# Kernel tuning notes

Measured on AMD Instinct MI355X. Metric: run time of the kernel, lower is better.

Reference implementation:

```python
import jax, jax.numpy as jnp
import numpy as np

NEG_SLOPE = 0.2
EPS = 1e-16

N_NODES = 10000
N_EDGES = 80000
F_IN = 128
HID = 300
H1 = 5  # first_heads
H3 = 3  # out_head
N_CLASSES = 40


def gat_conv(x, edge_index, W, att_src, att_dst, bias, heads, out_ch, concat):
    """PyG-style GATConv (v1 attention), eval mode (no dropout).

    x: [N, F_in]; edge_index: [2, E] (row 0 = source, row 1 = target),
    self-loops already included. W: [F_in, heads*out_ch];
    att_src/att_dst: [heads, out_ch].
    """
    N = x.shape[0]
    h = (x @ W).reshape(N, heads, out_ch)            # [N, H, C]
    a_src = jnp.einsum('nhc,hc->nh', h, att_src)     # [N, H]
    a_dst = jnp.einsum('nhc,hc->nh', h, att_dst)     # [N, H]
    src, dst = edge_index[0], edge_index[1]
    e = jax.nn.leaky_relu(a_src[src] + a_dst[dst], NEG_SLOPE)  # [E, H]
    # segment softmax over incoming edges of each target node
    m = jax.ops.segment_max(e, dst, num_segments=N)  # [N, H]
    ex = jnp.exp(e - m[dst])
    s = jax.ops.segment_sum(ex, dst, num_segments=N)
    alpha = ex / (s[dst] + EPS)                      # [E, H]
    msg = h[src] * alpha[:, :, None]                 # [E, H, C]
    out = jax.ops.segment_sum(msg, dst, num_segments=N)  # [N, H, C]
    if concat:
        out = out.reshape(N, heads * out_ch)
    else:
        out = out.mean(axis=1)
    return out + bias


def setup_inputs() -> dict:
    key = jax.random.key(0)
    ks = jax.random.split(key, 12)
    glorot = lambda k, shape: jax.random.normal(k, shape, jnp.float32) * np.sqrt(
        2.0 / (shape[0] + shape[-1]))
    x = jax.random.normal(ks[0], (N_NODES, F_IN), jnp.float32)
    edge_index = jax.random.randint(ks[1], (2, N_EDGES), 0, N_NODES, jnp.int64)
    return {
        'x': x,
        'edge_index': edge_index,
        'W1': glorot(ks[2], (F_IN, H1 * HID)),
        'as1': glorot(ks[3], (H1, HID)),
        'ad1': glorot(ks[4], (H1, HID)),
        'b1': jnp.zeros((H1 * HID,), jnp.float32),
        'W2': glorot(ks[5], (H1 * HID, H1 * HID)),
        'as2': glorot(ks[6], (H1, HID)),
        'ad2': glorot(ks[7], (H1, HID)),
        'b2': jnp.zeros((H1 * HID,), jnp.float32),
        'W3': glorot(ks[8], (H1 * HID, H3 * N_CLASSES)),
        'as3': glorot(ks[9], (H3, N_CLASSES)),
        'ad3': glorot(ks[10], (H3, N_CLASSES)),
        'b3': jnp.zeros((N_CLASSES,), jnp.float32),
    }


def reference(x, edge_index, W1, as1, ad1, b1, W2, as2, ad2, b2, W3, as3, ad3, b3):
    N = x.shape[0]
    # PyG GATConv adds self-loops by default
    loops = jnp.arange(N, dtype=edge_index.dtype)
    ei = jnp.concatenate([edge_index, jnp.stack([loops, loops])], axis=1)
    # dropout layers are identity in eval mode
    h = gat_conv(x, ei, W1, as1, ad1, b1, H1, HID, True)
    h = jax.nn.elu(h)
    h2 = gat_conv(h, ei, W2, as2, ad2, b2, H1, HID, True)
    h = jax.nn.elu(h + h2)
    h = gat_conv(h, ei, W3, as3, ad3, b3, H3, N_CLASSES, False)  # [N, n_cls]
    pooled = h.sum(axis=0, keepdims=True)                        # [1, n_cls]
    return (pooled, jax.nn.log_softmax(pooled, axis=1))
```

## Files before the change

### kernel.cpp

```cpp
#include <hip/hip_runtime.h>
#include <hip/hip_bf16.h>
#include <math.h>

#define NN       10000
#define F_IN     128
#define HID      300
#define H1       5
#define H3       3
#define NCLS     40
#define HC1      (H1*HID)
#define KPAD     1536
#define HS12     304
#define NL12     1520
#define HS3      48
#define NL3      144
#define LD3      160
#define NEG_SLOPE 0.2f
#define EPSV     1e-16f

typedef __attribute__((ext_vector_type(8))) short bf16x8;
typedef __attribute__((ext_vector_type(8))) unsigned short u16x8;
typedef __attribute__((ext_vector_type(4))) float f32x4;

__device__ inline unsigned short f2bf(float f) {
  unsigned int u = __builtin_bit_cast(unsigned int, f);
  unsigned int r = (u + 0x7FFFu + ((u >> 16) & 1u)) >> 16;
  return (unsigned short)r;
}
__device__ inline float bf2f(unsigned short s) {
  unsigned int u = ((unsigned int)s) << 16;
  return __builtin_bit_cast(float, u);
}

__device__ __forceinline__ void gl2lds16(const unsigned short* g, unsigned short* l) {
  __builtin_amdgcn_global_load_lds(
      (const __attribute__((address_space(1))) unsigned int*)(const void*)g,
      (__attribute__((address_space(3))) unsigned int*)(void*)l, 16, 0, 0);
}

__global__ void k_count(const int* __restrict__ ei, int* __restrict__ counts,
                        int E0, int Etot) {
  int e = blockIdx.x * 256 + threadIdx.x;
  if (e >= Etot) return;
  int dst = (e < E0) ? ei[E0 + e] : (e - E0);
  atomicAdd(&counts[dst], 1);
}

__global__ __launch_bounds__(256) void k_scan(const int* __restrict__ counts,
                                              int* __restrict__ offsets,
                                              int* __restrict__ cursor,
                                              int N, int Etot) {
  __shared__ int sh[256];
  const int CH = 40;
  int t = threadIdx.x;
  int base = t * CH;
  int s = 0;
  for (int i = 0; i < CH; i++) {
    int idx = base + i;
    if (idx < N) s += counts[idx];
  }
  sh[t] = s;
  __syncthreads();
  for (int d = 1; d < 256; d <<= 1) {
    int v = (t >= d) ? sh[t - d] : 0;
    __syncthreads();
    sh[t] += v;
    __syncthreads();
  }
  int run = sh[t] - s;
  for (int i = 0; i < CH; i++) {
    int idx = base + i;
    if (idx < N) {
      offsets[idx] = run;
      cursor[idx] = run;
      run += counts[idx];
    }
  }
  if (t == 0) offsets[N] = Etot;
}

__global__ void k_scatter(const int* __restrict__ ei, int* __restrict__ cursor,
                          int* __restrict__ csr_src, int E0, int Etot) {
  int e = blockIdx.x * 256 + threadIdx.x;
  if (e >= Etot) return;
  int src, dst;
  if (e < E0) { src = ei[e]; dst = ei[E0 + e]; }
  else        { src = dst = e - E0; }
  int pos = atomicAdd(&cursor[dst], 1);
  csr_src[pos] = src;
}

__global__ void k_cvt(const float* __restrict__ in, unsigned short* __restrict__ out,
                      int R, int C, int Cpad) {
  long long idx = (long long)blockIdx.x * 256 + threadIdx.x;
  if (idx >= (long long)R * Cpad) return;
  int r = (int)(idx / Cpad), c = (int)(idx - (long long)r * Cpad);
  out[idx] = (c < C) ? f2bf(in[(size_t)r * C + c]) : 0;
}

__global__ void k_attpad3(const float* __restrict__ as1, const float* __restrict__ ad1,
                          const float* __restrict__ as2, const float* __restrict__ ad2,
                          const float* __restrict__ as3, const float* __restrict__ ad3,
                          float* __restrict__ ps1, float* __restrict__ pd1,
                          float* __restrict__ ps2, float* __restrict__ pd2,
                          float* __restrict__ ps3, float* __restrict__ pd3) {
  int i = blockIdx.x * 256 + threadIdx.x;
  if (i < KPAD) {
    int h = i / HS12, cin = i - h * HS12;
    bool live = (h < H1) && (cin < HID);
    int o = live ? (h * HID + cin) : 0;
    ps1[i] = live ? as1[o] : 0.f;
    pd1[i] = live ? ad1[o] : 0.f;
    ps2[i] = live ? as2[o] : 0.f;
    pd2[i] = live ? ad2[o] : 0.f;
  }
  if (i < LD3) {
    int h = i / HS3, cin = i - h * HS3;
    bool live = (h < H3) && (cin < NCLS);
    ps3[i] = live ? as3[h * NCLS + cin] : 0.f;
    pd3[i] = live ? ad3[h * NCLS + cin] : 0.f;
  }
}

__global__ __launch_bounds__(256) void k_cvtT(const float* __restrict__ in,
                                              unsigned short* __restrict__ out,
                                              int K, int Nm, int kC, int kS, int Kp,
                                              int nC, int nS, int Nmp) {
  __shared__ float tile[64][65];
  int k0 = blockIdx.y * 64, n0 = blockIdx.x * 64;
  int c = threadIdx.x & 63, r = threadIdx.x >> 6;
  for (int rr = r; rr < 64; rr += 4) {
    int kp = k0 + rr;
    int np = n0 + c;
    float v = 0.f;
    if (kp < Kp && np < Nmp) {
      int ck = kp % kS, bk = kp / kS;
      int cn = np % nS, bn_ = np / nS;
      int ko = bk * kC + ck, no = bn_ * nC + cn;
      if (ck < kC && ko < K && cn < nC && no < Nm) v = in[(size_t)ko * Nm + no];
    }
    tile[rr][c] = v;
  }
  __syncthreads();
  for (int rr = r; rr < 64; rr += 4) {
    int np = n0 + rr, kp = k0 + c;
    if (np < Nmp && kp < Kp) out[(size_t)np * Kp + kp] = f2bf(tile[c][rr]);
  }
}

#define BM 128
#define BN 128
#define BK 64

__global__ __launch_bounds__(256) void gemm_mfma(
    const unsigned short* __restrict__ A,
    const unsigned short* __restrict__ Bt,
    unsigned short* __restrict__ Cbf,
    int M, int Kpad, int Nmat, int ldc, int klen,
    float* __restrict__ Cacc) {
  __shared__ unsigned short As[BM * BK];
  __shared__ unsigned short Bs[BN * BK];
  int tid = threadIdx.x;
  int lane = tid & 63, wid = tid >> 6;
  int wm = wid >> 1, wn = wid & 1;
  int bm = blockIdx.y * BM, bn = blockIdx.x * BN;
  int quad = lane >> 4, l16 = lane & 15;
  int kq = quad * 8;
  int koff = blockIdx.z * klen;

  int ar0 = min(bm + (2 * wid) * 16 + l16, M - 1);
  int ar1 = min(bm + (2 * wid + 1) * 16 + l16, M - 1);
  int br0 = min(bn + (2 * wid) * 16 + l16, Nmat - 1);
  int br1 = min(bn + (2 * wid + 1) * 16 + l16, Nmat - 1);
  const unsigned short* gA0 = A + (size_t)ar0 * Kpad + kq;
  const unsigned short* gA1 = A + (size_t)ar1 * Kpad + kq;
  const unsigned short* gB0 = Bt + (size_t)br0 * Kpad + kq;
  const unsigned short* gB1 = Bt + (size_t)br1 * Kpad + kq;
  unsigned short* lA = As + 4 * wid * 512;
  unsigned short* lB = Bs + 4 * wid * 512;

  f32x4 acc[4][4] = {};

  for (int kt = koff; kt < koff + klen; kt += BK) {
    gl2lds16(gA0 + kt,      lA);
    gl2lds16(gA0 + kt + 32, lA + 512);
    gl2lds16(gA1 + kt,      lA + 1024);
    gl2lds16(gA1 + kt + 32, lA + 1536);
    gl2lds16(gB0 + kt,      lB);
    gl2lds16(gB0 + kt + 32, lB + 512);
    gl2lds16(gB1 + kt,      lB + 1024);
    gl2lds16(gB1 + kt + 32, lB + 1536);
    __syncthreads();
#pragma unroll
    for (int kh = 0; kh < 2; kh++) {
      bf16x8 af[4], bfr[4];
#pragma unroll
      for (int i = 0; i < 4; i++) {
        af[i]  = *(const bf16x8*)(As + ((wm * 4 + i) * 2 + kh) * 512 + lane * 8);
        bfr[i] = *(const bf16x8*)(Bs + ((wn * 4 + i) * 2 + kh) * 512 + lane * 8);
      }
#pragma unroll
      for (int i = 0; i < 4; i++)
#pragma unroll
        for (int j = 0; j < 4; j++)
          acc[i][j] = __builtin_amdgcn_mfma_f32_16x16x32_bf16(af[i], bfr[j], acc[i][j], 0, 0, 0);
    }
    __syncthreads();
  }

#pragma unroll
  for (int i = 0; i < 4; i++) {
    int rowb = bm + wm * 64 + i * 16 + quad * 4;
#pragma unroll
    for (int j = 0; j < 4; j++) {
      int col = bn + wn * 64 + j * 16 + l16;
      if (col < ldc) {
        bool live = col < Nmat;
        if (Cacc) {
#pragma unroll
          for (int r = 0; r < 4; r++) {
            int row = rowb + r;
            if (live && row < M) atomicAdd(&Cacc[(size_t)row * ldc + col], acc[i][j][r]);
          }
        } else {
#pragma unroll
          for (int r = 0; r < 4; r++) {
            int row = rowb + r;
            if (row < M) Cbf[(size_t)row * ldc + col] = live ? f2bf(acc[i][j][r]) : 0;
          }
        }
      }
    }
  }
}

__global__ void k_c3(const float* __restrict__ Cacc, unsigned short* __restrict__ out,
                     int total) {
  int idx = blockIdx.x * 256 + threadIdx.x;
  if (idx >= total) return;
  int col = idx % LD3;
  out[idx] = (col < NL3) ? f2bf(Cacc[idx]) : 0;
}

__global__ void k_att(const unsigned short* __restrict__ hfeat, int ldh,
                      const float* __restrict__ attp_s,
                      const float* __restrict__ attp_d,
                      float* __restrict__ asrc, float* __restrict__ adst,
                      int H, int HS) {
  int n = blockIdx.x, t = threadIdx.x;
  __shared__ float s_ps[8], s_pd[8];
  if (t < 8) { s_ps[t] = 0.f; s_pd[t] = 0.f; }
  __syncthreads();
  int col0 = t * 8;
  if (col0 < ldh) {
    int hj = col0 / HS;
    u16x8 rv = *(const u16x8*)(hfeat + (size_t)n * ldh + col0);
    float ps = 0.f, pd = 0.f;
#pragma unroll
    for (int j = 0; j < 8; j++) {
      float v = bf2f(rv[j]);
      ps += v * attp_s[col0 + j];
      pd += v * attp_d[col0 + j];
    }
    atomicAdd(&s_ps[hj], ps);
    atomicAdd(&s_pd[hj], pd);
  }
  __syncthreads();
  if (t < H) {
    asrc[(size_t)n * H + t] = s_ps[t];
    adst[(size_t)n * H + t] = s_pd[t];
  }
}

__global__ void k_stats(const float* __restrict__ asrc,
                        const float* __restrict__ adst,
                        const int* __restrict__ csr_src,
                        const int* __restrict__ offsets,
                        float* __restrict__ alpha, int N, int H) {
  int t = blockIdx.x * 256 + threadIdx.x;
  if (t >= N * H) return;
  int n = t / H, h = t - n * H;
  int s0 = offsets[n], s1 = offsets[n + 1];
  float ad = adst[t];
  float m = -1e30f;
  for (int p = s0; p < s1; p++) {
    float v = asrc[csr_src[p] * H + h] + ad;
    v = v > 0.f ? v : NEG_SLOPE * v;
    m = fmaxf(m, v);
  }
  float sum = 0.f;
  for (int p = s0; p < s1; p++) {
    float v = asrc[csr_src[p] * H + h] + ad;
    v = v > 0.f ? v : NEG_SLOPE * v;
    float ex = expf(v - m);
    alpha[(size_t)p * 8 + h] = ex;
    sum += ex;
  }
  float r = 1.f / (sum + EPSV);
  for (int p = s0; p < s1; p++) alpha[(size_t)p * 8 + h] *= r;
}

__global__ __launch_bounds__(64) void k_agg(
    const unsigned short* __restrict__ hfeat, int ldh,
    const float* __restrict__ alpha,
    const int* __restrict__ csr_src,
    const int* __restrict__ offsets,
    const float* __restrict__ bias,
    const unsigned short* __restrict__ prevbf,
    unsigned short* __restrict__ out_bf,
    const float* __restrict__ b3,
    float* __restrict__ h3,
    int HS, int C, int H, int mode) {
  int n = blockIdx.x;
  int t = threadIdx.x;
  int s0 = offsets[n], s1 = offsets[n + 1];
  int col0 = blockIdx.y * 512 + t * 8;
  bool active = col0 < ldh;
  int hj = active ? (col0 / HS) : 0;
  int cbase = col0 - hj * HS;
  float acc[8] = {};

  __shared__ int s_src[64];
  __shared__ float s_alpha[64 * 8];
  __shared__ float s_out[LD3];

  for (int base = s0; base < s1; base += 64) {
    int chunk = min(64, s1 - base);
    if (t < chunk) s_src[t] = csr_src[base + t];
    for (int i = t; i < chunk * 8; i += 64) {
      int e = i >> 3, h = i & 7;
      s_alpha[i] = (h < H) ? alpha[(size_t)(base + e) * 8 + h] : 0.f;
    }
    __syncthreads();
    if (active) {
      u16x8 rv = *(const u16x8*)(hfeat + (size_t)s_src[0] * ldh + col0);
      for (int e = 0; e < chunk; e++) {
        u16x8 cur = rv;
        if (e + 1 < chunk)
          rv = *(const u16x8*)(hfeat + (size_t)s_src[e + 1] * ldh + col0);
        float al = s_alpha[e * 8 + hj];
#pragma unroll
        for (int j = 0; j < 8; j++) acc[j] += al * bf2f(cur[j]);
      }
    }
    __syncthreads();
  }

  if (mode == 2) {
    if (active) {
#pragma unroll
      for (int j = 0; j < 8; j++) s_out[col0 + j] = acc[j];
    }
    __syncthreads();
    if (t < NCLS)
      h3[(size_t)n * NCLS + t] =
          (s_out[t] + s_out[HS + t] + s_out[2 * HS + t]) * (1.f / 3.f) + b3[t];
    return;
  }

  if (!active) return;
#pragma unroll
  for (int j = 0; j < 8; j++) {
    int cin = cbase + j;
    bool live = (hj < H) && (cin < C);
    float v = 0.f;
    if (live) {
      v = acc[j] + bias[hj * C + cin];
      if (mode == 1) v += bf2f(prevbf[(size_t)n * ldh + col0 + j]);
      v = v > 0.f ? v : (expf(v) - 1.f);
    }
    out_bf[(size_t)n * ldh + col0 + j] = live ? f2bf(v) : 0;
  }
}

__global__ void k_pool(const float* __restrict__ h3, float* __restrict__ pooled,
                       int N) {
  int col = threadIdx.x;
  if (col >= NCLS) return;
  int row = blockIdx.x * 4 + threadIdx.y;
  int stride = gridDim.x * 4;
  float acc = 0.f;
  for (int r = row; r < N; r += stride) acc += h3[(size_t)r * NCLS + col];
  atomicAdd(&pooled[col], acc);
}

__global__ __launch_bounds__(64) void k_final(const float* __restrict__ pooled,
                                              float* __restrict__ out) {
  int t = threadIdx.x;
  float v = (t < NCLS) ? pooled[t] : -INFINITY;
  float m = v;
  for (int o = 32; o > 0; o >>= 1) m = fmaxf(m, __shfl_xor(m, o));
  float ex = (t < NCLS) ? expf(v - m) : 0.f;
  float s = ex;
  for (int o = 32; o > 0; o >>= 1) s += __shfl_xor(s, o);
  float lse = m + logf(s);
  if (t < NCLS) {
    out[t] = v;
    out[NCLS + t] = v - lse;
  }
}

extern "C" void kernel_launch(void* const* d_in, const int* in_sizes, int n_in,
                              void* d_out, int out_size, void* d_ws, size_t ws_size,
                              hipStream_t stream) {
  const float* x   = (const float*)d_in[0];
  const int*   ei  = (const int*)d_in[1];
  const float* W1  = (const float*)d_in[2];
  const float* as1 = (const float*)d_in[3];
  const float* ad1 = (const float*)d_in[4];
  const float* b1  = (const float*)d_in[5];
  const float* W2  = (const float*)d_in[6];
  const float* as2 = (const float*)d_in[7];
  const float* ad2 = (const float*)d_in[8];
  const float* b2  = (const float*)d_in[9];
  const float* W3  = (const float*)d_in[10];
  const float* as3 = (const float*)d_in[11];
  const float* ad3 = (const float*)d_in[12];
  const float* b3  = (const float*)d_in[13];
  float* out = (float*)d_out;

  const int N = NN;
  const int E0 = in_sizes[1] / 2;
  const int Etot = E0 + N;

  float* f = (float*)d_ws;
  float* asrc   = f;
  float* adst   = asrc + (size_t)N * H1;
  float* alphab = adst + (size_t)N * H1;
  float* pooled = alphab + (size_t)Etot * 8;
  float* h3     = pooled + 64;
  float* attps1 = h3 + (size_t)N * NCLS;
  float* attpd1 = attps1 + KPAD;
  float* attps2 = attpd1 + KPAD;
  float* attpd2 = attps2 + KPAD;
  float* attps3 = attpd2 + KPAD;
  float* attpd3 = attps3 + LD3;
  float* Cacc   = attpd3 + LD3;
  int* counts  = (int*)(Cacc + (size_t)N * LD3);
  int* offsets = counts + N;
  int* cursor  = offsets + N + 1;
  int* csr_src = cursor + N;
  uintptr_t pp = (uintptr_t)(csr_src + Etot);
  pp = (pp + 15) & ~(uintptr_t)15;
  unsigned short* hfbf = (unsigned short*)pp;
  unsigned short* abf  = hfbf + (size_t)N * KPAD;
  unsigned short* btbf = abf + (size_t)N * KPAD;

  hipMemsetAsync(counts, 0, (size_t)N * sizeof(int), stream);
  hipMemsetAsync(pooled, 0, 64 * sizeof(float), stream);

  k_count<<<(Etot + 255) / 256, 256, 0, stream>>>(ei, counts, E0, Etot);
  k_scan<<<1, 256, 0, stream>>>(counts, offsets, cursor, N, Etot);
  k_scatter<<<(Etot + 255) / 256, 256, 0, stream>>>(ei, cursor, csr_src, E0, Etot);
  k_attpad3<<<(KPAD + 255) / 256, 256, 0, stream>>>(as1, ad1, as2, ad2, as3, ad3,
                                                    attps1, attpd1, attps2, attpd2,
                                                    attps3, attpd3);

  {
    k_cvt<<<((long long)N * F_IN + 255) / 256, 256, 0, stream>>>(x, abf, N, F_IN, F_IN);
    dim3 tg((NL12 + 63) / 64, (F_IN + 63) / 64);
    k_cvtT<<<tg, 256, 0, stream>>>(W1, btbf, F_IN, HC1, F_IN, F_IN, F_IN, HID, HS12, NL12);
    dim3 grid((NL12 + BN - 1) / BN, (N + BM - 1) / BM);
    gemm_mfma<<<grid, 256, 0, stream>>>(abf, btbf, hfbf, N, F_IN, NL12, KPAD, F_IN, nullptr);
    k_att<<<N, 192, 0, stream>>>(hfbf, KPAD, attps1, attpd1, asrc, adst, H1, HS12);
    k_stats<<<(N * H1 + 255) / 256, 256, 0, stream>>>(asrc, adst, csr_src, offsets,
                                                      alphab, N, H1);
    k_agg<<<dim3(N, 3), 64, 0, stream>>>(hfbf, KPAD, alphab, csr_src, offsets, b1,
                                         nullptr, abf, nullptr, nullptr,
                                         HS12, HID, H1, 0);
  }

  {
    dim3 tg((NL12 + 63) / 64, KPAD / 64);
    k_cvtT<<<tg, 256, 0, stream>>>(W2, btbf, HC1, HC1, HID, HS12, KPAD, HID, HS12, NL12);
    dim3 grid((NL12 + BN - 1) / BN, (N + BM - 1) / BM);
    gemm_mfma<<<grid, 256, 0, stream>>>(abf, btbf, hfbf, N, KPAD, NL12, KPAD, KPAD, nullptr);
    k_att<<<N, 192, 0, stream>>>(hfbf, KPAD, attps2, attpd2, asrc, adst, H1, HS12);
    k_stats<<<(N * H1 + 255) / 256, 256, 0, stream>>>(asrc, adst, csr_src, offsets,
                                                      alphab, N, H1);
    k_agg<<<dim3(N, 3), 64, 0, stream>>>(hfbf, KPAD, alphab, csr_src, offsets, b2,
                                         abf, abf, nullptr, nullptr,
                                         HS12, HID, H1, 1);
  }

  {
    dim3 tg((NL3 + 63) / 64, KPAD / 64);
    k_cvtT<<<tg, 256, 0, stream>>>(W3, btbf, HC1, H3 * NCLS, HID, HS12, KPAD, NCLS, HS3, NL3);
    hipMemsetAsync(Cacc, 0, (size_t)N * LD3 * sizeof(float), stream);
    dim3 grid((LD3 + BN - 1) / BN, (N + BM - 1) / BM, 4);
    gemm_mfma<<<grid, 256, 0, stream>>>(abf, btbf, nullptr, N, KPAD, NL3, LD3,
                                        KPAD / 4, Cacc);
    k_c3<<<((N * LD3) + 255) / 256, 256, 0, stream>>>(Cacc, hfbf, N * LD3);
    k_att<<<N, 64, 0, stream>>>(hfbf, LD3, attps3, attpd3, asrc, adst, H3, HS3);
    k_stats<<<(N * H3 + 255) / 256, 256, 0, stream>>>(asrc, adst, csr_src, offsets,
                                                      alphab, N, H3);
    k_agg<<<dim3(N, 1), 64, 0, stream>>>(hfbf, LD3, alphab, csr_src, offsets, nullptr,
                                         nullptr, nullptr, b3, h3,
                                         HS3, NCLS, H3, 2);
  }

  k_pool<<<64, dim3(64, 4), 0, stream>>>(h3, pooled, N);
  k_final<<<1, 64, 0, stream>>>(pooled, out);
}
```

Before: 600.9 us.

## Enlarge GEMM row tile to 256 with 8 waves and fuse layer-3 convert into k_att

The MFMA GEMM block now covers 256 rows instead of 128 and runs 512 threads (8 waves). Each wave loads 32 rows of A and 16 rows of B into LDS, so the block's 128-column B tile is reused over twice as many rows. Separately, the k_c3 kernel that turned the split-K fp32 accumulator into bf16 is removed. k_att now reads the fp32 buffer directly, writes the bf16 features and computes the attention dot products in one pass, saving a launch and a pass over the data. The trade-off is fewer, larger blocks (more LDS per block), which may lower occupancy and leave tail imbalance on the small grids.

New measurement: 579.3 us. 1.04x faster.

```diff
diff --git a/kernel.cpp b/kernel.cpp
--- a/kernel.cpp
+++ b/kernel.cpp
@@ -148,11 +148,11 @@
   }
 }
 
-#define BM 128
+#define BM 256
 #define BN 128
 #define BK 64
 
-__global__ __launch_bounds__(256) void gemm_mfma(
+__global__ __launch_bounds__(512) void gemm_mfma(
     const unsigned short* __restrict__ A,
     const unsigned short* __restrict__ Bt,
     unsigned short* __restrict__ Cbf,
@@ -168,16 +168,14 @@
   int kq = quad * 8;
   int koff = blockIdx.z * klen;
 
-  int ar0 = min(bm + (2 * wid) * 16 + l16, M - 1);
-  int ar1 = min(bm + (2 * wid + 1) * 16 + l16, M - 1);
-  int br0 = min(bn + (2 * wid) * 16 + l16, Nmat - 1);
-  int br1 = min(bn + (2 * wid + 1) * 16 + l16, Nmat - 1);
+  int ar0 = min(bm + 32 * wid + l16, M - 1);
+  int ar1 = min(bm + 32 * wid + 16 + l16, M - 1);
+  int br0 = min(bn + 16 * wid + l16, Nmat - 1);
   const unsigned short* gA0 = A + (size_t)ar0 * Kpad + kq;
   const unsigned short* gA1 = A + (size_t)ar1 * Kpad + kq;
   const unsigned short* gB0 = Bt + (size_t)br0 * Kpad + kq;
-  const unsigned short* gB1 = Bt + (size_t)br1 * Kpad + kq;
   unsigned short* lA = As + 4 * wid * 512;
-  unsigned short* lB = Bs + 4 * wid * 512;
+  unsigned short* lB = Bs + 2 * wid * 512;
 
   f32x4 acc[4][4] = {};
 
@@ -188,8 +186,6 @@
     gl2lds16(gA1 + kt + 32, lA + 1536);
     gl2lds16(gB0 + kt,      lB);
     gl2lds16(gB0 + kt + 32, lB + 512);
-    gl2lds16(gB1 + kt,      lB + 1024);
-    gl2lds16(gB1 + kt + 32, lB + 1536);
     __syncthreads();
 #pragma unroll
     for (int kh = 0; kh < 2; kh++) {
@@ -234,19 +230,11 @@
   }
 }
 
-__global__ void k_c3(const float* __restrict__ Cacc, unsigned short* __restrict__ out,
-                     int total) {
-  int idx = blockIdx.x * 256 + threadIdx.x;
-  if (idx >= total) return;
-  int col = idx % LD3;
-  out[idx] = (col < NL3) ? f2bf(Cacc[idx]) : 0;
-}
-
-__global__ void k_att(const unsigned short* __restrict__ hfeat, int ldh,
+__global__ void k_att(unsigned short* __restrict__ hfeat, int ldh,
                       const float* __restrict__ attp_s,
                       const float* __restrict__ attp_d,
                       float* __restrict__ asrc, float* __restrict__ adst,
-                      int H, int HS) {
+                      int H, int HS, const float* __restrict__ Cacc, int Nlive) {
   int n = blockIdx.x, t = threadIdx.x;
   __shared__ float s_ps[8], s_pd[8];
   if (t < 8) { s_ps[t] = 0.f; s_pd[t] = 0.f; }
@@ -254,13 +242,29 @@
   int col0 = t * 8;
   if (col0 < ldh) {
     int hj = col0 / HS;
-    u16x8 rv = *(const u16x8*)(hfeat + (size_t)n * ldh + col0);
     float ps = 0.f, pd = 0.f;
-#pragma unroll
-    for (int j = 0; j < 8; j++) {
-      float v = bf2f(rv[j]);
-      ps += v * attp_s[col0 + j];
-      pd += v * attp_d[col0 + j];
+    if (Cacc) {
+      const float4* p = (const float4*)(Cacc + (size_t)n * ldh + col0);
+      float4 f0 = p[0], f1 = p[1];
+      float fv[8] = {f0.x, f0.y, f0.z, f0.w, f1.x, f1.y, f1.z, f1.w};
+      u16x8 st;
+#pragma unroll
+      for (int j = 0; j < 8; j++) {
+        bool live = (col0 + j) < Nlive;
+        float v = live ? fv[j] : 0.f;
+        st[j] = live ? f2bf(v) : 0;
+        ps += v * attp_s[col0 + j];
+        pd += v * attp_d[col0 + j];
+      }
+      *(u16x8*)(hfeat + (size_t)n * ldh + col0) = st;
+    } else {
+      u16x8 rv = *(const u16x8*)(hfeat + (size_t)n * ldh + col0);
+#pragma unroll
+      for (int j = 0; j < 8; j++) {
+        float v = bf2f(rv[j]);
+        ps += v * attp_s[col0 + j];
+        pd += v * attp_d[col0 + j];
+      }
     }
     atomicAdd(&s_ps[hj], ps);
     atomicAdd(&s_pd[hj], pd);
@@ -461,8 +465,9 @@
     dim3 tg((NL12 + 63) / 64, (F_IN + 63) / 64);
     k_cvtT<<<tg, 256, 0, stream>>>(W1, btbf, F_IN, HC1, F_IN, F_IN, F_IN, HID, HS12, NL12);
     dim3 grid((NL12 + BN - 1) / BN, (N + BM - 1) / BM);
-    gemm_mfma<<<grid, 256, 0, stream>>>(abf, btbf, hfbf, N, F_IN, NL12, KPAD, F_IN, nullptr);
-    k_att<<<N, 192, 0, stream>>>(hfbf, KPAD, attps1, attpd1, asrc, adst, H1, HS12);
+    gemm_mfma<<<grid, 512, 0, stream>>>(abf, btbf, hfbf, N, F_IN, NL12, KPAD, F_IN, nullptr);
+    k_att<<<N, 192, 0, stream>>>(hfbf, KPAD, attps1, attpd1, asrc, adst, H1, HS12,
+                                 nullptr, 0);
     k_stats<<<(N * H1 + 255) / 256, 256, 0, stream>>>(asrc, adst, csr_src, offsets,
                                                       alphab, N, H1);
     k_agg<<<dim3(N, 3), 64, 0, stream>>>(hfbf, KPAD, alphab, csr_src, offsets, b1,
@@ -474,8 +479,9 @@
     dim3 tg((NL12 + 63) / 64, KPAD / 64);
     k_cvtT<<<tg, 256, 0, stream>>>(W2, btbf, HC1, HC1, HID, HS12, KPAD, HID, HS12, NL12);
     dim3 grid((NL12 + BN - 1) / BN, (N + BM - 1) / BM);
-    gemm_mfma<<<grid, 256, 0, stream>>>(abf, btbf, hfbf, N, KPAD, NL12, KPAD, KPAD, nullptr);
-    k_att<<<N, 192, 0, stream>>>(hfbf, KPAD, attps2, attpd2, asrc, adst, H1, HS12);
+    gemm_mfma<<<grid, 512, 0, stream>>>(abf, btbf, hfbf, N, KPAD, NL12, KPAD, KPAD, nullptr);
+    k_att<<<N, 192, 0, stream>>>(hfbf, KPAD, attps2, attpd2, asrc, adst, H1, HS12,
+                                 nullptr, 0);
     k_stats<<<(N * H1 + 255) / 256, 256, 0, stream>>>(asrc, adst, csr_src, offsets,
                                                       alphab, N, H1);
     k_agg<<<dim3(N, 3), 64, 0, stream>>>(hfbf, KPAD, alphab, csr_src, offsets, b2,
@@ -488,10 +494,10 @@
     k_cvtT<<<tg, 256, 0, stream>>>(W3, btbf, HC1, H3 * NCLS, HID, HS12, KPAD, NCLS, HS3, NL3);
     hipMemsetAsync(Cacc, 0, (size_t)N * LD3 * sizeof(float), stream);
     dim3 grid((LD3 + BN - 1) / BN, (N + BM - 1) / BM, 4);
-    gemm_mfma<<<grid, 256, 0, stream>>>(abf, btbf, nullptr, N, KPAD, NL3, LD3,
+    gemm_mfma<<<grid, 512, 0, stream>>>(abf, btbf, nullptr, N, KPAD, NL3, LD3,
                                         KPAD / 4, Cacc);
-    k_c3<<<((N * LD3) + 255) / 256, 256, 0, stream>>>(Cacc, hfbf, N * LD3);
-    k_att<<<N, 64, 0, stream>>>(hfbf, LD3, attps3, attpd3, asrc, adst, H3, HS3);
+    k_att<<<N, 64, 0, stream>>>(hfbf, LD3, attps3, attpd3, asrc, adst, H3, HS3,
+                                Cacc, NL3);
     k_stats<<<(N * H3 + 255) / 256, 256, 0, stream>>>(asrc, adst, csr_src, offsets,
                                                       alphab, N, H3);
     k_agg<<<dim3(N, 1), 64, 0, stream>>>(hfbf, LD3, alphab, csr_src, offsets, nullptr,
```
